# Performance work log

Measured on AMD Instinct MI355X. Metric: run time of the kernel, lower is better.

## Reference

```python
import jax, jax.numpy as jnp
import numpy as np

N_EMBD = 1568  # 2 * 784
EPS = 1e-5


def layernorm(x, g, b):
    mu = jnp.mean(x, axis=-1, keepdims=True)
    var = jnp.var(x, axis=-1, keepdims=True)
    return (x - mu) * jax.lax.rsqrt(var + EPS) * g + b


def setup_inputs() -> dict:
    key = jax.random.key(0)
    ks = jax.random.split(key, 8)
    B, D, H, HS, FF, OUT = 1024, N_EMBD, 16, 98, 4 * N_EMBD, N_EMBD // 2
    s = 0.02
    return {
        "x": jax.random.normal(ks[0], (B, D), jnp.float32),
        "Wq": jax.random.normal(ks[1], (H, D, HS), jnp.float32) * s,
        "Wk": jax.random.normal(ks[2], (H, D, HS), jnp.float32) * s,
        "Wv": jax.random.normal(ks[3], (H, D, HS), jnp.float32) * s,
        "Wo": jax.random.normal(ks[4], (D, D), jnp.float32) * s,
        "bo": jnp.zeros((D,), jnp.float32),
        "g1": jnp.ones((D,), jnp.float32),
        "b1": jnp.zeros((D,), jnp.float32),
        "g2": jnp.ones((D,), jnp.float32),
        "b2": jnp.zeros((D,), jnp.float32),
        "W1": jax.random.normal(ks[5], (D, FF), jnp.float32) * s,
        "b1f": jnp.zeros((FF,), jnp.float32),
        "W2": jax.random.normal(ks[6], (FF, OUT), jnp.float32) * s,
        "b2f": jnp.zeros((OUT,), jnp.float32),
    }


def reference(x, Wq, Wk, Wv, Wo, bo, g1, b1, g2, b2, W1, b1f, W2, b2f):
    B, D = x.shape
    h = layernorm(x, g1, b1)                       # (B, D)
    # all 16 heads batched: per-head QKV projections
    q = jnp.einsum('bd,hde->bhe', h, Wq)           # (B, H, 98)
    k = jnp.einsum('bd,hde->bhe', h, Wk)
    v = jnp.einsum('bd,hde->bhe', h, Wv)
    # outer-product pseudo-attention, scaled by N**-0.5 with N = n_embd
    attn = jnp.einsum('bhi,bhj->bhij', q, k) * (D ** -0.5)  # (B, H, 98, 98)
    attn = jax.nn.softmax(attn, axis=-1)
    out = jnp.einsum('bhij,bhj->bhi', attn, v)     # (B, H, 98)
    out = out.reshape(B, D)                        # concat heads
    out = out @ Wo + bo                            # output proj (dropout = identity in eval)
    h2 = layernorm(out, g2, b2)
    ff = jax.nn.gelu(h2 @ W1 + b1f, approximate=False) @ W2 + b2f  # (B, 784)
    return ff
```

## Files before the change

kernel.cpp:

```cpp
#include <hip/hip_runtime.h>
#include <math.h>

#define B_ROWS 1024
#define D_EMB  1568
#define KP     1600
#define H_HEADS 16
#define HSZ    98
#define FF_DIM 6272
#define OUT_DIM 784

typedef unsigned short ushort_t;
typedef __attribute__((ext_vector_type(8))) short short8;
typedef __attribute__((ext_vector_type(4))) float floatx4;

static __device__ __forceinline__ ushort_t f2bf(float f) {
    unsigned int u = __builtin_bit_cast(unsigned int, f);
    u = (u + 0x7fffu + ((u >> 16) & 1u)) >> 16;
    return (ushort_t)u;
}
static __device__ __forceinline__ float bf2f(ushort_t h) {
    unsigned int u = ((unsigned int)h) << 16;
    return __builtin_bit_cast(float, u);
}

static __device__ __forceinline__ void load16_to_lds(const void* g, void* l) {
    __builtin_amdgcn_global_load_lds(
        (const __attribute__((address_space(1))) void*)g,
        (__attribute__((address_space(3))) void*)l,
        16, 0, 0);
}

__global__ __launch_bounds__(256) void ln_kernel(const float* __restrict__ x,
                                                 const float* __restrict__ g,
                                                 const float* __restrict__ b,
                                                 ushort_t* __restrict__ out,
                                                 int D, int DPAD) {
    const int row = blockIdx.x;
    const float* xr = x + (size_t)row * D;
    ushort_t* orow = out + (size_t)row * DPAD;

    float s = 0.f, s2 = 0.f;
    for (int i = threadIdx.x; i < D; i += blockDim.x) {
        float v = xr[i];
        s += v; s2 += v * v;
    }
    #pragma unroll
    for (int off = 32; off > 0; off >>= 1) {
        s  += __shfl_down(s,  off, 64);
        s2 += __shfl_down(s2, off, 64);
    }
    __shared__ float ws_[8], ws2_[8];
    const int wave = threadIdx.x >> 6, lane = threadIdx.x & 63;
    if (lane == 0) { ws_[wave] = s; ws2_[wave] = s2; }
    __syncthreads();
    if (threadIdx.x == 0) {
        float ts = 0.f, ts2 = 0.f;
        for (int i = 0; i < 4; i++) { ts += ws_[i]; ts2 += ws2_[i]; }
        ws_[0] = ts; ws2_[0] = ts2;
    }
    __syncthreads();
    const float mean = ws_[0] / (float)D;
    const float var  = ws2_[0] / (float)D - mean * mean;
    const float inv  = rsqrtf(var + 1e-5f);
    for (int i = threadIdx.x; i < DPAD; i += blockDim.x)
        orow[i] = (i < D) ? f2bf((xr[i] - mean) * inv * g[i] + b[i]) : (ushort_t)0;
}

static __device__ __forceinline__ void transpose_tile(const float* __restrict__ src,
                                                      ushort_t* __restrict__ dst,
                                                      int srcN, int Kvalid,
                                                      int k0, int n0,
                                                      int Nvalid, int Npad,
                                                      int dstride, int dbase) {
    __shared__ float t[64][65];
    const int tid = threadIdx.x;
    const int tx = tid & 63, ty = tid >> 6;
    #pragma unroll
    for (int r = 0; r < 16; r++) {
        const int kl = ty + r * 4;
        const int k = k0 + kl, n = n0 + tx;
        t[tx][kl] = (k < Kvalid && n < Nvalid) ? src[(size_t)k * srcN + n] : 0.f;
    }
    __syncthreads();
    #pragma unroll
    for (int w = 0; w < 4; w++) {
        const int nl = (tid >> 4) + w * 16;
        const int kc = (tid & 15) * 4;
        const int n = n0 + nl, k = k0 + kc;
        if (n < Npad && k < Kvalid) {
            ushort4 uv;
            uv.x = f2bf(t[nl][kc + 0]);
            uv.y = f2bf(t[nl][kc + 1]);
            uv.z = f2bf(t[nl][kc + 2]);
            uv.w = f2bf(t[nl][kc + 3]);
            *(ushort4*)(dst + (size_t)(dbase + n) * dstride + k) = uv;
        }
    }
}

__global__ __launch_bounds__(256) void prep1_kernel(const float* __restrict__ Wq,
                                                    const float* __restrict__ Wk,
                                                    const float* __restrict__ Wv,
                                                    const float* __restrict__ Wo,
                                                    ushort_t* __restrict__ qkvt,
                                                    ushort_t* __restrict__ Wot) {
    const int id = blockIdx.x;
    if (id < 2400) {
        const int ktile = id % 25;
        const int rest  = id / 25;
        const int ntile = rest & 1;
        const int hw    = rest >> 1;
        const int head  = hw & 15;
        const int which = hw >> 4;
        const float* src = (which == 0) ? Wq : (which == 1) ? Wk : Wv;
        src += (size_t)head * D_EMB * HSZ;
        transpose_tile(src, qkvt, HSZ, D_EMB, ktile * 64, ntile * 64,
                       HSZ, HSZ, KP, which * D_EMB + head * HSZ);
    } else {
        const int id2 = id - 2400;
        const int ktile = id2 % 25;
        const int ntile = id2 / 25;
        transpose_tile(Wo, Wot, D_EMB, D_EMB, ktile * 64, ntile * 64,
                       D_EMB, 1664, KP, 0);
    }
}

__global__ __launch_bounds__(256) void prep2_kernel(const float* __restrict__ W1,
                                                    const float* __restrict__ W2,
                                                    ushort_t* __restrict__ W1t,
                                                    ushort_t* __restrict__ W2t) {
    const int id = blockIdx.x;
    if (id < 2450) {
        const int ktile = id % 25;
        const int ntile = id / 25;
        transpose_tile(W1, W1t, FF_DIM, D_EMB, ktile * 64, ntile * 64,
                       FF_DIM, FF_DIM, KP, 0);
    } else {
        const int id2 = id - 2450;
        const int ktile = id2 % 98;
        const int ntile = id2 / 98;
        transpose_tile(W2, W2t, OUT_DIM, FF_DIM, ktile * 64, ntile * 64,
                       OUT_DIM, 896, FF_DIM, 0);
    }
}

template <int EPI>
__global__ __launch_bounds__(256) void gemm_bf16(const ushort_t* __restrict__ A,
                                                 const ushort_t* __restrict__ Bt,
                                                 ushort_t* __restrict__ P,
                                                 const float* __restrict__ bias,
                                                 int N, int Kstride, int nkTot) {
    __shared__ __align__(16) ushort_t As[2 * 128 * 32];
    __shared__ __align__(16) ushort_t Bs[2 * 128 * 32];

    const int tid  = threadIdx.x;
    const int wave = tid >> 6, lane = tid & 63;
    const int quad = lane >> 4, l16 = lane & 15;
    const int m0 = blockIdx.x * 128;
    const int n0 = blockIdx.y * 128;
    const int z = blockIdx.z, Z = gridDim.z;
    const int it0 = (int)((long long)nkTot * z / Z);
    const int it1 = (int)((long long)nkTot * (z + 1) / Z);

    const int srow = lane >> 2;
    const int scol = (lane & 3) << 3;
    const int wm = wave & 1, wn = wave >> 1;

    floatx4 acc[4][4] = {};

    for (int it = it0; it < it1; ++it) {
        const int k0 = it << 6;
        #pragma unroll
        for (int c = 0; c < 2; ++c) {
            const int rg = wave * 2 + c;
            const int row = rg * 16 + srow;
            #pragma unroll
            for (int ks = 0; ks < 2; ++ks) {
                load16_to_lds(A  + (size_t)(m0 + row) * Kstride + k0 + ks * 32 + scol,
                              &As[ks * 4096 + rg * 512]);
                load16_to_lds(Bt + (size_t)(n0 + row) * Kstride + k0 + ks * 32 + scol,
                              &Bs[ks * 4096 + rg * 512]);
            }
        }
        __syncthreads();

        #pragma unroll
        for (int ks = 0; ks < 2; ++ks) {
            short8 af[4], bfr[4];
            #pragma unroll
            for (int i = 0; i < 4; i++)
                af[i] = *(const short8*)&As[ks * 4096 + (wm * 64 + i * 16 + l16) * 32 + quad * 8];
            #pragma unroll
            for (int j = 0; j < 4; j++)
                bfr[j] = *(const short8*)&Bs[ks * 4096 + (wn * 64 + j * 16 + l16) * 32 + quad * 8];
            #pragma unroll
            for (int i = 0; i < 4; i++)
                #pragma unroll
                for (int j = 0; j < 4; j++)
                    acc[i][j] = __builtin_amdgcn_mfma_f32_16x16x32_bf16(af[i], bfr[j], acc[i][j], 0, 0, 0);
        }
        __syncthreads();
    }

    ushort_t* Pz = (EPI == 0) ? (P + (size_t)z * B_ROWS * N) : P;
    #pragma unroll
    for (int i = 0; i < 4; i++) {
        const int rbase = m0 + wm * 64 + i * 16 + quad * 4;
        #pragma unroll
        for (int j = 0; j < 4; j++) {
            const int col = n0 + wn * 64 + j * 16 + l16;
            if (col < N) {
                #pragma unroll
                for (int r = 0; r < 4; r++) {
                    float v = acc[i][j][r];
                    if (EPI == 1) {
                        v += bias[col];
                        v = 0.5f * v * (1.f + erff(v * 0.70710678118654752f));
                    }
                    Pz[(size_t)(rbase + r) * N + col] = f2bf(v);
                }
            }
        }
    }
}

template <int Z>
__global__ __launch_bounds__(256) void combine_ln_kernel(const ushort_t* __restrict__ P,
                                                         const float* __restrict__ bias,
                                                         const float* __restrict__ g,
                                                         const float* __restrict__ b,
                                                         ushort_t* __restrict__ out,
                                                         int N, int NPAD) {
    __shared__ float t[D_EMB];
    __shared__ float ws_[8], ws2_[8];
    const int row = blockIdx.x;
    const size_t plane = (size_t)B_ROWS * N;
    const ushort_t* Pr = P + (size_t)row * N;
    const int half = N >> 1;

    float s = 0.f, s2 = 0.f;
    for (int i = threadIdx.x; i < half; i += blockDim.x) {
        float v0 = bias[2 * i], v1 = bias[2 * i + 1];
        #pragma unroll
        for (int zz = 0; zz < Z; zz++) {
            const ushort2 u = *(const ushort2*)(Pr + (size_t)zz * plane + 2 * i);
            v0 += bf2f(u.x); v1 += bf2f(u.y);
        }
        t[2 * i] = v0; t[2 * i + 1] = v1;
        s += v0 + v1; s2 += v0 * v0 + v1 * v1;
    }
    #pragma unroll
    for (int off = 32; off > 0; off >>= 1) {
        s  += __shfl_down(s,  off, 64);
        s2 += __shfl_down(s2, off, 64);
    }
    const int wave = threadIdx.x >> 6, lane = threadIdx.x & 63;
    if (lane == 0) { ws_[wave] = s; ws2_[wave] = s2; }
    __syncthreads();
    if (threadIdx.x == 0) {
        float ts = 0.f, ts2 = 0.f;
        for (int i = 0; i < 4; i++) { ts += ws_[i]; ts2 += ws2_[i]; }
        ws_[0] = ts; ws2_[0] = ts2;
    }
    __syncthreads();
    const float mean = ws_[0] / (float)N;
    const float var  = ws2_[0] / (float)N - mean * mean;
    const float inv  = rsqrtf(var + 1e-5f);
    ushort_t* orow = out + (size_t)row * NPAD;
    for (int i = threadIdx.x; i < NPAD; i += blockDim.x)
        orow[i] = (i < N) ? f2bf((t[i] - mean) * inv * g[i] + b[i]) : (ushort_t)0;
}

template <int Z>
__global__ __launch_bounds__(256) void combine_out_kernel(const ushort_t* __restrict__ P,
                                                          const float* __restrict__ bias,
                                                          float* __restrict__ out, int N) {
    const int c2 = blockIdx.x * 256 + threadIdx.x;
    if (c2 >= (N >> 1)) return;
    const int row = blockIdx.y;
    const size_t plane = (size_t)B_ROWS * N;
    const size_t off = (size_t)row * N + 2 * c2;
    float v0 = bias[2 * c2], v1 = bias[2 * c2 + 1];
    #pragma unroll
    for (int zz = 0; zz < Z; zz++) {
        const ushort2 u = *(const ushort2*)(P + (size_t)zz * plane + off);
        v0 += bf2f(u.x); v1 += bf2f(u.y);
    }
    out[off] = v0; out[off + 1] = v1;
}

__global__ __launch_bounds__(128) void attn_kernel(const ushort_t* __restrict__ P,
                                                   ushort_t* __restrict__ out) {
    const int bh = blockIdx.x;
    const int b = bh >> 4, h = bh & 15;
    const size_t base = (size_t)b * 4704 + h * HSZ;
    const size_t plane = (size_t)B_ROWS * 4704;

    __shared__ float ks[HSZ], vs[HSZ];
    __shared__ float kmax_s, kmin_s;

    const int t = threadIdx.x;
    if (t < HSZ) {
        ks[t] = bf2f(P[base + 1568 + t]) + bf2f(P[plane + base + 1568 + t]);
        vs[t] = bf2f(P[base + 3136 + t]) + bf2f(P[plane + base + 3136 + t]);
    }
    __syncthreads();
    if (t == 0) {
        float mx = -1e30f, mn = 1e30f;
        for (int j = 0; j < HSZ; j++) { mx = fmaxf(mx, ks[j]); mn = fminf(mn, ks[j]); }
        kmax_s = mx; kmin_s = mn;
    }
    __syncthreads();
    if (t < HSZ) {
        const float q = bf2f(P[base + t]) + bf2f(P[plane + base + t]);
        const float ti = q * 0.025253813613805268f;
        const float m = (ti >= 0.f) ? ti * kmax_s : ti * kmin_s;
        float s = 0.f, acc = 0.f;
        for (int j = 0; j < HSZ; j++) {
            const float e = __expf(ti * ks[j] - m);
            s += e; acc += e * vs[j];
        }
        out[(size_t)b * KP + h * HSZ + t] = f2bf(acc / s);
    }
}

extern "C" void kernel_launch(void* const* d_in, const int* in_sizes, int n_in,
                              void* d_out, int out_size, void* d_ws, size_t ws_size,
                              hipStream_t stream) {
    const float* x   = (const float*)d_in[0];
    const float* Wq  = (const float*)d_in[1];
    const float* Wk  = (const float*)d_in[2];
    const float* Wv  = (const float*)d_in[3];
    const float* Wo  = (const float*)d_in[4];
    const float* bo  = (const float*)d_in[5];
    const float* g1  = (const float*)d_in[6];
    const float* b1  = (const float*)d_in[7];
    const float* g2  = (const float*)d_in[8];
    const float* b2  = (const float*)d_in[9];
    const float* W1  = (const float*)d_in[10];
    const float* b1f = (const float*)d_in[11];
    const float* W2  = (const float*)d_in[12];
    const float* b2f = (const float*)d_in[13];
    float* out = (float*)d_out;

    char* w = (char*)d_ws;
    ushort_t* qkvt = (ushort_t*)(w);
    ushort_t* Wot  = (ushort_t*)(w + 15155200);
    ushort_t* W1t  = (ushort_t*)(w);
    ushort_t* Pw2  = (ushort_t*)(w);
    ushort_t* Pb   = (ushort_t*)(w + 20480000);
    ushort_t* ff1  = (ushort_t*)(w + 20480000);
    ushort_t* W2t  = (ushort_t*)(w + 33325056);
    ushort_t* h_bf = (ushort_t*)(w + 47775744);

    ln_kernel<<<B_ROWS, 256, 0, stream>>>(x, g1, b1, h_bf, D_EMB, KP);

    prep1_kernel<<<3050, 256, 0, stream>>>(Wq, Wk, Wv, Wo, qkvt, Wot);

    gemm_bf16<0><<<dim3(8, 37, 2), 256, 0, stream>>>(h_bf, qkvt, Pb, nullptr, 4704, KP, 25);

    attn_kernel<<<B_ROWS * H_HEADS, 128, 0, stream>>>(Pb, h_bf);

    gemm_bf16<0><<<dim3(8, 13, 4), 256, 0, stream>>>(h_bf, Wot, Pb, nullptr, D_EMB, KP, 25);

    combine_ln_kernel<4><<<B_ROWS, 256, 0, stream>>>(Pb, bo, g2, b2, h_bf, D_EMB, KP);

    prep2_kernel<<<3822, 256, 0, stream>>>(W1, W2, W1t, W2t);

    gemm_bf16<1><<<dim3(8, 49, 1), 256, 0, stream>>>(h_bf, W1t, ff1, b1f, FF_DIM, KP, 25);

    gemm_bf16<0><<<dim3(8, 7, 9), 256, 0, stream>>>(ff1, W2t, Pw2, nullptr, OUT_DIM, FF_DIM, 98);

    combine_out_kernel<9><<<dim3(2, B_ROWS), 256, 0, stream>>>(Pw2, b2f, out, OUT_DIM);
}
```

Before: 351.7 us.

## Replace LDS-staged GEMM with direct global-to-register MFMA loads and drop K padding

The GEMM no longer stages A and B tiles through LDS with global_load_lds and barriers. Each wave now loads its own MFMA fragments straight from global memory with a K step of 32, and the loop is unrolled by 2. The K padding to 1600 is removed so every buffer uses stride 1568, and the W1/W2 transposes are split into separate launches, with workspace offsets rearranged to match. This removes LDS traffic and synchronization, but gives up data reuse between waves in a block, so it leans on L2/L1 for A/B reuse and on uncoalesced 16-byte row-strided loads.

```diff
diff --git a/kernel.cpp b/kernel.cpp
--- a/kernel.cpp
+++ b/kernel.cpp
@@ -3,7 +3,6 @@
 
 #define B_ROWS 1024
 #define D_EMB  1568
-#define KP     1600
 #define H_HEADS 16
 #define HSZ    98
 #define FF_DIM 6272
@@ -23,21 +22,13 @@
     return __builtin_bit_cast(float, u);
 }
 
-static __device__ __forceinline__ void load16_to_lds(const void* g, void* l) {
-    __builtin_amdgcn_global_load_lds(
-        (const __attribute__((address_space(1))) void*)g,
-        (__attribute__((address_space(3))) void*)l,
-        16, 0, 0);
-}
-
 __global__ __launch_bounds__(256) void ln_kernel(const float* __restrict__ x,
                                                  const float* __restrict__ g,
                                                  const float* __restrict__ b,
-                                                 ushort_t* __restrict__ out,
-                                                 int D, int DPAD) {
+                                                 ushort_t* __restrict__ out, int D) {
     const int row = blockIdx.x;
     const float* xr = x + (size_t)row * D;
-    ushort_t* orow = out + (size_t)row * DPAD;
+    ushort_t* orow = out + (size_t)row * D;
 
     float s = 0.f, s2 = 0.f;
     for (int i = threadIdx.x; i < D; i += blockDim.x) {
@@ -62,8 +53,8 @@
     const float mean = ws_[0] / (float)D;
     const float var  = ws2_[0] / (float)D - mean * mean;
     const float inv  = rsqrtf(var + 1e-5f);
-    for (int i = threadIdx.x; i < DPAD; i += blockDim.x)
-        orow[i] = (i < D) ? f2bf((xr[i] - mean) * inv * g[i] + b[i]) : (ushort_t)0;
+    for (int i = threadIdx.x; i < D; i += blockDim.x)
+        orow[i] = f2bf((xr[i] - mean) * inv * g[i] + b[i]);
 }
 
 static __device__ __forceinline__ void transpose_tile(const float* __restrict__ src,
@@ -115,100 +106,71 @@
         const float* src = (which == 0) ? Wq : (which == 1) ? Wk : Wv;
         src += (size_t)head * D_EMB * HSZ;
         transpose_tile(src, qkvt, HSZ, D_EMB, ktile * 64, ntile * 64,
-                       HSZ, HSZ, KP, which * D_EMB + head * HSZ);
+                       HSZ, HSZ, D_EMB, which * D_EMB + head * HSZ);
     } else {
         const int id2 = id - 2400;
         const int ktile = id2 % 25;
         const int ntile = id2 / 25;
         transpose_tile(Wo, Wot, D_EMB, D_EMB, ktile * 64, ntile * 64,
-                       D_EMB, 1664, KP, 0);
-    }
-}
-
-__global__ __launch_bounds__(256) void prep2_kernel(const float* __restrict__ W1,
-                                                    const float* __restrict__ W2,
-                                                    ushort_t* __restrict__ W1t,
-                                                    ushort_t* __restrict__ W2t) {
-    const int id = blockIdx.x;
-    if (id < 2450) {
-        const int ktile = id % 25;
-        const int ntile = id / 25;
-        transpose_tile(W1, W1t, FF_DIM, D_EMB, ktile * 64, ntile * 64,
-                       FF_DIM, FF_DIM, KP, 0);
-    } else {
-        const int id2 = id - 2450;
-        const int ktile = id2 % 98;
-        const int ntile = id2 / 98;
-        transpose_tile(W2, W2t, OUT_DIM, FF_DIM, ktile * 64, ntile * 64,
-                       OUT_DIM, 896, FF_DIM, 0);
-    }
+                       D_EMB, 1664, D_EMB, 0);
+    }
+}
+
+__global__ __launch_bounds__(256) void transpose_plain(const float* __restrict__ src,
+                                                       ushort_t* __restrict__ dst,
+                                                       int K, int N, int Npad) {
+    transpose_tile(src, dst, N, K, blockIdx.y * 64, blockIdx.x * 64, N, Npad, K, 0);
 }
 
 template <int EPI>
-__global__ __launch_bounds__(256) void gemm_bf16(const ushort_t* __restrict__ A,
-                                                 const ushort_t* __restrict__ Bt,
-                                                 ushort_t* __restrict__ P,
-                                                 const float* __restrict__ bias,
-                                                 int N, int Kstride, int nkTot) {
-    __shared__ __align__(16) ushort_t As[2 * 128 * 32];
-    __shared__ __align__(16) ushort_t Bs[2 * 128 * 32];
-
+__global__ __launch_bounds__(256) void gemm_direct(const ushort_t* __restrict__ A,
+                                                   const ushort_t* __restrict__ Bt,
+                                                   ushort_t* __restrict__ P,
+                                                   const float* __restrict__ bias,
+                                                   int N, int K, int nkTot) {
     const int tid  = threadIdx.x;
     const int wave = tid >> 6, lane = tid & 63;
     const int quad = lane >> 4, l16 = lane & 15;
-    const int m0 = blockIdx.x * 128;
-    const int n0 = blockIdx.y * 128;
+    const int wm = wave & 1, wn = wave >> 1;
+    const int m0 = blockIdx.x * 128 + wm * 64;
+    const int n0 = blockIdx.y * 128 + wn * 64;
     const int z = blockIdx.z, Z = gridDim.z;
     const int it0 = (int)((long long)nkTot * z / Z);
     const int it1 = (int)((long long)nkTot * (z + 1) / Z);
 
-    const int srow = lane >> 2;
-    const int scol = (lane & 3) << 3;
-    const int wm = wave & 1, wn = wave >> 1;
+    const ushort_t* arow[4];
+    const ushort_t* brow[4];
+    #pragma unroll
+    for (int i = 0; i < 4; i++)
+        arow[i] = A + (size_t)(m0 + i * 16 + l16) * K + quad * 8;
+    #pragma unroll
+    for (int j = 0; j < 4; j++)
+        brow[j] = Bt + (size_t)(n0 + j * 16 + l16) * K + quad * 8;
 
     floatx4 acc[4][4] = {};
 
+    #pragma unroll 2
     for (int it = it0; it < it1; ++it) {
-        const int k0 = it << 6;
-        #pragma unroll
-        for (int c = 0; c < 2; ++c) {
-            const int rg = wave * 2 + c;
-            const int row = rg * 16 + srow;
-            #pragma unroll
-            for (int ks = 0; ks < 2; ++ks) {
-                load16_to_lds(A  + (size_t)(m0 + row) * Kstride + k0 + ks * 32 + scol,
-                              &As[ks * 4096 + rg * 512]);
-                load16_to_lds(Bt + (size_t)(n0 + row) * Kstride + k0 + ks * 32 + scol,
-                              &Bs[ks * 4096 + rg * 512]);
-            }
-        }
-        __syncthreads();
-
-        #pragma unroll
-        for (int ks = 0; ks < 2; ++ks) {
-            short8 af[4], bfr[4];
-            #pragma unroll
-            for (int i = 0; i < 4; i++)
-                af[i] = *(const short8*)&As[ks * 4096 + (wm * 64 + i * 16 + l16) * 32 + quad * 8];
+        const int k = it << 5;
+        short8 af[4], bfr[4];
+        #pragma unroll
+        for (int i = 0; i < 4; i++) af[i]  = *(const short8*)(arow[i] + k);
+        #pragma unroll
+        for (int j = 0; j < 4; j++) bfr[j] = *(const short8*)(brow[j] + k);
+        #pragma unroll
+        for (int i = 0; i < 4; i++)
             #pragma unroll
             for (int j = 0; j < 4; j++)
-                bfr[j] = *(const short8*)&Bs[ks * 4096 + (wn * 64 + j * 16 + l16) * 32 + quad * 8];
-            #pragma unroll
-            for (int i = 0; i < 4; i++)
-                #pragma unroll
-                for (int j = 0; j < 4; j++)
-                    acc[i][j] = __builtin_amdgcn_mfma_f32_16x16x32_bf16(af[i], bfr[j], acc[i][j], 0, 0, 0);
-        }
-        __syncthreads();
+                acc[i][j] = __builtin_amdgcn_mfma_f32_16x16x32_bf16(af[i], bfr[j], acc[i][j], 0, 0, 0);
     }
 
     ushort_t* Pz = (EPI == 0) ? (P + (size_t)z * B_ROWS * N) : P;
     #pragma unroll
     for (int i = 0; i < 4; i++) {
-        const int rbase = m0 + wm * 64 + i * 16 + quad * 4;
+        const int rbase = m0 + i * 16 + quad * 4;
         #pragma unroll
         for (int j = 0; j < 4; j++) {
-            const int col = n0 + wn * 64 + j * 16 + l16;
+            const int col = n0 + j * 16 + l16;
             if (col < N) {
                 #pragma unroll
                 for (int r = 0; r < 4; r++) {
@@ -229,8 +191,7 @@
                                                          const float* __restrict__ bias,
                                                          const float* __restrict__ g,
                                                          const float* __restrict__ b,
-                                                         ushort_t* __restrict__ out,
-                                                         int N, int NPAD) {
+                                                         ushort_t* __restrict__ out, int N) {
     __shared__ float t[D_EMB];
     __shared__ float ws_[8], ws2_[8];
     const int row = blockIdx.x;
@@ -266,9 +227,9 @@
     const float mean = ws_[0] / (float)N;
     const float var  = ws2_[0] / (float)N - mean * mean;
     const float inv  = rsqrtf(var + 1e-5f);
-    ushort_t* orow = out + (size_t)row * NPAD;
-    for (int i = threadIdx.x; i < NPAD; i += blockDim.x)
-        orow[i] = (i < N) ? f2bf((t[i] - mean) * inv * g[i] + b[i]) : (ushort_t)0;
+    ushort_t* orow = out + (size_t)row * N;
+    for (int i = threadIdx.x; i < N; i += blockDim.x)
+        orow[i] = f2bf((t[i] - mean) * inv * g[i] + b[i]);
 }
 
 template <int Z>
@@ -320,7 +281,7 @@
             const float e = __expf(ti * ks[j] - m);
             s += e; acc += e * vs[j];
         }
-        out[(size_t)b * KP + h * HSZ + t] = f2bf(acc / s);
+        out[(size_t)b * D_EMB + h * HSZ + t] = f2bf(acc / s);
     }
 }
 
@@ -345,31 +306,33 @@
 
     char* w = (char*)d_ws;
     ushort_t* qkvt = (ushort_t*)(w);
-    ushort_t* Wot  = (ushort_t*)(w + 15155200);
+    ushort_t* Wot  = (ushort_t*)(w + 14852096);
     ushort_t* W1t  = (ushort_t*)(w);
-    ushort_t* Pw2  = (ushort_t*)(w);
-    ushort_t* Pb   = (ushort_t*)(w + 20480000);
-    ushort_t* ff1  = (ushort_t*)(w + 20480000);
-    ushort_t* W2t  = (ushort_t*)(w + 33325056);
-    ushort_t* h_bf = (ushort_t*)(w + 47775744);
-
-    ln_kernel<<<B_ROWS, 256, 0, stream>>>(x, g1, b1, h_bf, D_EMB, KP);
+    ushort_t* W2t  = (ushort_t*)(w);
+    ushort_t* Pb   = (ushort_t*)(w + 20070400);
+    ushort_t* ff1  = (ushort_t*)(w + 20070400);
+    ushort_t* Pw2  = (ushort_t*)(w + 32915456);
+    ushort_t* h_bf = (ushort_t*)(w + 48168960);
+
+    ln_kernel<<<B_ROWS, 256, 0, stream>>>(x, g1, b1, h_bf, D_EMB);
 
     prep1_kernel<<<3050, 256, 0, stream>>>(Wq, Wk, Wv, Wo, qkvt, Wot);
 
-    gemm_bf16<0><<<dim3(8, 37, 2), 256, 0, stream>>>(h_bf, qkvt, Pb, nullptr, 4704, KP, 25);
+    gemm_direct<0><<<dim3(8, 37, 2), 256, 0, stream>>>(h_bf, qkvt, Pb, nullptr, 4704, D_EMB, 49);
 
     attn_kernel<<<B_ROWS * H_HEADS, 128, 0, stream>>>(Pb, h_bf);
 
-    gemm_bf16<0><<<dim3(8, 13, 4), 256, 0, stream>>>(h_bf, Wot, Pb, nullptr, D_EMB, KP, 25);
-
-    combine_ln_kernel<4><<<B_ROWS, 256, 0, stream>>>(Pb, bo, g2, b2, h_bf, D_EMB, KP);
-
-    prep2_kernel<<<3822, 256, 0, stream>>>(W1, W2, W1t, W2t);
-
-    gemm_bf16<1><<<dim3(8, 49, 1), 256, 0, stream>>>(h_bf, W1t, ff1, b1f, FF_DIM, KP, 25);
-
-    gemm_bf16<0><<<dim3(8, 7, 9), 256, 0, stream>>>(ff1, W2t, Pw2, nullptr, OUT_DIM, FF_DIM, 98);
+    gemm_direct<0><<<dim3(8, 13, 4), 256, 0, stream>>>(h_bf, Wot, Pb, nullptr, D_EMB, D_EMB, 49);
+
+    combine_ln_kernel<4><<<B_ROWS, 256, 0, stream>>>(Pb, bo, g2, b2, h_bf, D_EMB);
+
+    transpose_plain<<<dim3(98, 25), 256, 0, stream>>>(W1, W1t, D_EMB, FF_DIM, FF_DIM);
+
+    gemm_direct<1><<<dim3(8, 49, 1), 256, 0, stream>>>(h_bf, W1t, ff1, b1f, FF_DIM, D_EMB, 49);
+
+    transpose_plain<<<dim3(14, 98), 256, 0, stream>>>(W2, W2t, FF_DIM, OUT_DIM, 896);
+
+    gemm_direct<0><<<dim3(8, 7, 9), 256, 0, stream>>>(ff1, W2t, Pw2, nullptr, OUT_DIM, FF_DIM, 196);
 
     combine_out_kernel<9><<<dim3(2, B_ROWS), 256, 0, stream>>>(Pw2, b2f, out, OUT_DIM);
 }
```

After: 440.2 us. +25.2%, slower.

## Merge independent prep/LN kernels and swizzle GEMM block order for L2 locality

Applied to the files above, without the earlier changes.

The first layernorm is folded into the QKV/Wo weight-transpose kernel, and the combine+layernorm is folded into the W1/W2 transpose kernel. Each merged kernel uses block-index ranges to run both pieces of work in one launch, removing two launches and letting independent work overlap. The GEMMs move to a 1D grid with a swizzled mapping, so each group of 64 blocks covers an 8x8 patch of M and N/split tiles, which should improve L2 reuse of A and B. Padding blocks return early. The merged kernels now mix tasks of different shapes, and the first one puts the LDS arrays of both paths in one kernel.

```diff
diff --git a/kernel.cpp b/kernel.cpp
--- a/kernel.cpp
+++ b/kernel.cpp
@@ -30,15 +30,11 @@
         16, 0, 0);
 }
 
-__global__ __launch_bounds__(256) void ln_kernel(const float* __restrict__ x,
-                                                 const float* __restrict__ g,
-                                                 const float* __restrict__ b,
-                                                 ushort_t* __restrict__ out,
-                                                 int D, int DPAD) {
-    const int row = blockIdx.x;
-    const float* xr = x + (size_t)row * D;
-    ushort_t* orow = out + (size_t)row * DPAD;
-
+static __device__ void ln_row(const float* __restrict__ xr,
+                              const float* __restrict__ g,
+                              const float* __restrict__ b,
+                              ushort_t* __restrict__ orow, int D, int DPAD) {
+    __shared__ float ws_[8], ws2_[8];
     float s = 0.f, s2 = 0.f;
     for (int i = threadIdx.x; i < D; i += blockDim.x) {
         float v = xr[i];
@@ -49,7 +45,6 @@
         s  += __shfl_down(s,  off, 64);
         s2 += __shfl_down(s2, off, 64);
     }
-    __shared__ float ws_[8], ws2_[8];
     const int wave = threadIdx.x >> 6, lane = threadIdx.x & 63;
     if (lane == 0) { ws_[wave] = s; ws2_[wave] = s2; }
     __syncthreads();
@@ -98,16 +93,23 @@
     }
 }
 
-__global__ __launch_bounds__(256) void prep1_kernel(const float* __restrict__ Wq,
-                                                    const float* __restrict__ Wk,
-                                                    const float* __restrict__ Wv,
-                                                    const float* __restrict__ Wo,
-                                                    ushort_t* __restrict__ qkvt,
-                                                    ushort_t* __restrict__ Wot) {
+__global__ __launch_bounds__(256) void prep1x_kernel(const float* __restrict__ x,
+                                                     const float* __restrict__ g1,
+                                                     const float* __restrict__ b1,
+                                                     const float* __restrict__ Wq,
+                                                     const float* __restrict__ Wk,
+                                                     const float* __restrict__ Wv,
+                                                     const float* __restrict__ Wo,
+                                                     ushort_t* __restrict__ h_bf,
+                                                     ushort_t* __restrict__ qkvt,
+                                                     ushort_t* __restrict__ Wot) {
     const int id = blockIdx.x;
-    if (id < 2400) {
-        const int ktile = id % 25;
-        const int rest  = id / 25;
+    if (id < 1024) {
+        ln_row(x + (size_t)id * D_EMB, g1, b1, h_bf + (size_t)id * KP, D_EMB, KP);
+    } else if (id < 3424) {
+        const int t = id - 1024;
+        const int ktile = t % 25;
+        const int rest  = t / 25;
         const int ntile = rest & 1;
         const int hw    = rest >> 1;
         const int head  = hw & 15;
@@ -117,51 +119,38 @@
         transpose_tile(src, qkvt, HSZ, D_EMB, ktile * 64, ntile * 64,
                        HSZ, HSZ, KP, which * D_EMB + head * HSZ);
     } else {
-        const int id2 = id - 2400;
-        const int ktile = id2 % 25;
-        const int ntile = id2 / 25;
+        const int t = id - 3424;
+        const int ktile = t % 25;
+        const int ntile = t / 25;
         transpose_tile(Wo, Wot, D_EMB, D_EMB, ktile * 64, ntile * 64,
                        D_EMB, 1664, KP, 0);
     }
 }
 
-__global__ __launch_bounds__(256) void prep2_kernel(const float* __restrict__ W1,
-                                                    const float* __restrict__ W2,
-                                                    ushort_t* __restrict__ W1t,
-                                                    ushort_t* __restrict__ W2t) {
-    const int id = blockIdx.x;
-    if (id < 2450) {
-        const int ktile = id % 25;
-        const int ntile = id / 25;
-        transpose_tile(W1, W1t, FF_DIM, D_EMB, ktile * 64, ntile * 64,
-                       FF_DIM, FF_DIM, KP, 0);
-    } else {
-        const int id2 = id - 2450;
-        const int ktile = id2 % 98;
-        const int ntile = id2 / 98;
-        transpose_tile(W2, W2t, OUT_DIM, FF_DIM, ktile * 64, ntile * 64,
-                       OUT_DIM, 896, FF_DIM, 0);
-    }
-}
-
 template <int EPI>
-__global__ __launch_bounds__(256) void gemm_bf16(const ushort_t* __restrict__ A,
-                                                 const ushort_t* __restrict__ Bt,
-                                                 ushort_t* __restrict__ P,
-                                                 const float* __restrict__ bias,
-                                                 int N, int Kstride, int nkTot) {
+__global__ __launch_bounds__(256) void gemm_lds(const ushort_t* __restrict__ A,
+                                                const ushort_t* __restrict__ Bt,
+                                                ushort_t* __restrict__ P,
+                                                const float* __restrict__ bias,
+                                                int N, int Kstride, int nkTot,
+                                                int NT, int Z) {
     __shared__ __align__(16) ushort_t As[2 * 128 * 32];
     __shared__ __align__(16) ushort_t Bs[2 * 128 * 32];
+
+    const int id = blockIdx.x;
+    const int nz = (id & 7) + ((id >> 6) << 3);
+    if (nz >= NT * Z) return;
+    const int mq = (id >> 3) & 7;
+    const int z  = nz / NT;
+    const int nt = nz - z * NT;
+    const int m0 = mq * 128;
+    const int n0 = nt * 128;
+    const int it0 = (int)((long long)nkTot * z / Z);
+    const int it1 = (int)((long long)nkTot * (z + 1) / Z);
 
     const int tid  = threadIdx.x;
     const int wave = tid >> 6, lane = tid & 63;
     const int quad = lane >> 4, l16 = lane & 15;
-    const int m0 = blockIdx.x * 128;
-    const int n0 = blockIdx.y * 128;
-    const int z = blockIdx.z, Z = gridDim.z;
-    const int it0 = (int)((long long)nkTot * z / Z);
-    const int it1 = (int)((long long)nkTot * (z + 1) / Z);
-
     const int srow = lane >> 2;
     const int scol = (lane & 3) << 3;
     const int wm = wave & 1, wn = wave >> 1;
@@ -225,15 +214,14 @@
 }
 
 template <int Z>
-__global__ __launch_bounds__(256) void combine_ln_kernel(const ushort_t* __restrict__ P,
-                                                         const float* __restrict__ bias,
-                                                         const float* __restrict__ g,
-                                                         const float* __restrict__ b,
-                                                         ushort_t* __restrict__ out,
-                                                         int N, int NPAD) {
+static __device__ void combine_ln_row(const ushort_t* __restrict__ P,
+                                      const float* __restrict__ bias,
+                                      const float* __restrict__ g,
+                                      const float* __restrict__ b,
+                                      ushort_t* __restrict__ out,
+                                      int row, int N, int NPAD) {
     __shared__ float t[D_EMB];
     __shared__ float ws_[8], ws2_[8];
-    const int row = blockIdx.x;
     const size_t plane = (size_t)B_ROWS * N;
     const ushort_t* Pr = P + (size_t)row * N;
     const int half = N >> 1;
@@ -269,6 +257,33 @@
     ushort_t* orow = out + (size_t)row * NPAD;
     for (int i = threadIdx.x; i < NPAD; i += blockDim.x)
         orow[i] = (i < N) ? f2bf((t[i] - mean) * inv * g[i] + b[i]) : (ushort_t)0;
+}
+
+__global__ __launch_bounds__(256) void mid_kernel(const ushort_t* __restrict__ P,
+                                                  const float* __restrict__ bo,
+                                                  const float* __restrict__ g2,
+                                                  const float* __restrict__ b2,
+                                                  ushort_t* __restrict__ h_bf,
+                                                  const float* __restrict__ W1,
+                                                  const float* __restrict__ W2,
+                                                  ushort_t* __restrict__ W1t,
+                                                  ushort_t* __restrict__ W2t) {
+    const int id = blockIdx.x;
+    if (id < 1024) {
+        combine_ln_row<4>(P, bo, g2, b2, h_bf, id, D_EMB, KP);
+    } else if (id < 3474) {
+        const int t = id - 1024;
+        const int ktile = t % 25;
+        const int ntile = t / 25;
+        transpose_tile(W1, W1t, FF_DIM, D_EMB, ktile * 64, ntile * 64,
+                       FF_DIM, FF_DIM, KP, 0);
+    } else {
+        const int t = id - 3474;
+        const int ktile = t % 98;
+        const int ntile = t / 98;
+        transpose_tile(W2, W2t, OUT_DIM, FF_DIM, ktile * 64, ntile * 64,
+                       OUT_DIM, 896, FF_DIM, 0);
+    }
 }
 
 template <int Z>
@@ -351,25 +366,21 @@
     ushort_t* Pb   = (ushort_t*)(w + 20480000);
     ushort_t* ff1  = (ushort_t*)(w + 20480000);
     ushort_t* W2t  = (ushort_t*)(w + 33325056);
-    ushort_t* h_bf = (ushort_t*)(w + 47775744);
-
-    ln_kernel<<<B_ROWS, 256, 0, stream>>>(x, g1, b1, h_bf, D_EMB, KP);
-
-    prep1_kernel<<<3050, 256, 0, stream>>>(Wq, Wk, Wv, Wo, qkvt, Wot);
-
-    gemm_bf16<0><<<dim3(8, 37, 2), 256, 0, stream>>>(h_bf, qkvt, Pb, nullptr, 4704, KP, 25);
+    ushort_t* h_bf = (ushort_t*)(w + 48103424);
+
+    prep1x_kernel<<<4074, 256, 0, stream>>>(x, g1, b1, Wq, Wk, Wv, Wo, h_bf, qkvt, Wot);
+
+    gemm_lds<0><<<640, 256, 0, stream>>>(h_bf, qkvt, Pb, nullptr, 4704, KP, 25, 37, 2);
 
     attn_kernel<<<B_ROWS * H_HEADS, 128, 0, stream>>>(Pb, h_bf);
 
-    gemm_bf16<0><<<dim3(8, 13, 4), 256, 0, stream>>>(h_bf, Wot, Pb, nullptr, D_EMB, KP, 25);
-
-    combine_ln_kernel<4><<<B_ROWS, 256, 0, stream>>>(Pb, bo, g2, b2, h_bf, D_EMB, KP);
-
-    prep2_kernel<<<3822, 256, 0, stream>>>(W1, W2, W1t, W2t);
-
-    gemm_bf16<1><<<dim3(8, 49, 1), 256, 0, stream>>>(h_bf, W1t, ff1, b1f, FF_DIM, KP, 25);
-
-    gemm_bf16<0><<<dim3(8, 7, 9), 256, 0, stream>>>(ff1, W2t, Pw2, nullptr, OUT_DIM, FF_DIM, 98);
+    gemm_lds<0><<<448, 256, 0, stream>>>(h_bf, Wot, Pb, nullptr, D_EMB, KP, 25, 13, 4);
+
+    mid_kernel<<<4846, 256, 0, stream>>>(Pb, bo, g2, b2, h_bf, W1, W2, W1t, W2t);
+
+    gemm_lds<1><<<448, 256, 0, stream>>>(h_bf, W1t, ff1, b1f, FF_DIM, KP, 25, 49, 1);
+
+    gemm_lds<0><<<512, 256, 0, stream>>>(ff1, W2t, Pw2, nullptr, OUT_DIM, FF_DIM, 98, 7, 9);
 
     combine_out_kernel<9><<<dim3(2, B_ROWS), 256, 0, stream>>>(Pw2, b2f, out, OUT_DIM);
 }
```

New measurement: 329.8 us. -6.2%, faster.
